# Kernel optimization log

Measured on AMD Instinct MI355X. Metric: run time of the kernel, lower is better.

Reference implementation:

```python
import jax, jax.numpy as jnp
import numpy as np

EMBED_DIM = 1280
NUM_HEADS = 20
HEAD_DIM = EMBED_DIM // NUM_HEADS
ENC_LEN = 8192
SCALE = float(HEAD_DIM ** -0.5)


def setup_inputs() -> dict:
    key = jax.random.key(0)
    ks = jax.random.split(key, 7)
    s = 0.02
    return {
        "hidden_states": jax.random.normal(ks[0], (1, 1, EMBED_DIM), dtype=jnp.float32),
        "cross_k_cache": jax.random.normal(ks[1], (1, NUM_HEADS, ENC_LEN, HEAD_DIM), dtype=jnp.float32),
        "cross_v_cache": jax.random.normal(ks[2], (1, NUM_HEADS, ENC_LEN, HEAD_DIM), dtype=jnp.float32),
        "q_w": jax.random.normal(ks[3], (EMBED_DIM, EMBED_DIM), dtype=jnp.float32) * s,
        "q_b": jax.random.normal(ks[4], (EMBED_DIM,), dtype=jnp.float32) * s,
        "out_w": jax.random.normal(ks[5], (EMBED_DIM, EMBED_DIM), dtype=jnp.float32) * s,
        "out_b": jax.random.normal(ks[6], (EMBED_DIM,), dtype=jnp.float32) * s,
    }


def reference(hidden_states, cross_k_cache, cross_v_cache, q_w, q_b, out_w, out_b):
    # q_proj (torch Linear: x @ W.T + b), then scale
    q = hidden_states @ q_w.T + q_b                       # [1,1,E]
    q = q * jnp.asarray(SCALE, q.dtype)
    q = q.reshape(1, 1, NUM_HEADS, HEAD_DIM).transpose(0, 2, 1, 3)  # [1,H,1,Dh]
    # attention scores over cached keys: [1,H,1,L]
    attn = jnp.einsum("bhqd,bhld->bhql", q, cross_k_cache)
    attn = jax.nn.softmax(attn, axis=-1)
    # weighted sum of values: [1,H,1,Dh]
    out = jnp.einsum("bhql,bhld->bhqd", attn, cross_v_cache)
    out = out.transpose(0, 2, 1, 3).reshape(1, 1, EMBED_DIM)
    return out @ out_w.T + out_b
```

## Files before the change

### kernel.cpp

```cpp
#include <hip/hip_runtime.h>
#include <math.h>

#define EMBED 1280
#define NHEAD 20
#define HDIM 64
#define LENC 8192
#define CHUNK 128
#define NBLK (LENC / CHUNK)
#define NREC 256
#define PREC 72
#define QSCALE 0.125f

__global__ __launch_bounds__(256) void matvec_row(
    const float* __restrict__ W, const float* __restrict__ x,
    const float* __restrict__ b, float* __restrict__ y, float scale) {
  int row = blockIdx.x;
  int t = threadIdx.x;
  int w = t >> 6, lane = t & 63;
  const float4* Wr = reinterpret_cast<const float4*>(W + (size_t)row * EMBED);
  const float4* x4 = reinterpret_cast<const float4*>(x);
  float4 wv = Wr[t], xv = x4[t];
  float acc = wv.x * xv.x + wv.y * xv.y + wv.z * xv.z + wv.w * xv.w;
  if (t < 64) {
    float4 wv2 = Wr[256 + t], xv2 = x4[256 + t];
    acc += wv2.x * xv2.x + wv2.y * xv2.y + wv2.z * xv2.z + wv2.w * xv2.w;
  }
#pragma unroll
  for (int msk = 32; msk > 0; msk >>= 1) acc += __shfl_xor(acc, msk);
  __shared__ float red[4];
  if (lane == 0) red[w] = acc;
  __syncthreads();
  if (t == 0) y[row] = scale * (red[0] + red[1] + red[2] + red[3] + b[row]);
}

__global__ __launch_bounds__(256) void attn_partial(
    const float* __restrict__ K, const float* __restrict__ V,
    const float* __restrict__ q, float* __restrict__ part) {
  int blk = blockIdx.x;
  int h = blk / NBLK;
  int c = blk % NBLK;
  int tid = threadIdx.x;
  int w = tid >> 6;
  int lane = tid & 63;
  int grp = lane >> 4;
  int l16 = lane & 15;

  size_t row0 = (size_t)c * CHUNK + (size_t)w * 32;
  const float4* Kh4 = reinterpret_cast<const float4*>(K + (size_t)h * LENC * HDIM) + row0 * 16;
  const float4* Vh4 = reinterpret_cast<const float4*>(V + (size_t)h * LENC * HDIM) + row0 * 16;
  float4 qv = reinterpret_cast<const float4*>(q + h * HDIM)[l16];

  float4 kreg[8], vreg[8];
#pragma unroll
  for (int it = 0; it < 8; ++it) kreg[it] = Kh4[(it * 4 + grp) * 16 + l16];
#pragma unroll
  for (int it = 0; it < 8; ++it) vreg[it] = Vh4[(it * 4 + grp) * 16 + l16];

  float s[8];
#pragma unroll
  for (int it = 0; it < 8; ++it) {
    float t = kreg[it].x * qv.x + kreg[it].y * qv.y + kreg[it].z * qv.z + kreg[it].w * qv.w;
    t += __shfl_xor(t, 1);
    t += __shfl_xor(t, 2);
    t += __shfl_xor(t, 4);
    t += __shfl_xor(t, 8);
    s[it] = t;
  }

  float m = s[0];
#pragma unroll
  for (int it = 1; it < 8; ++it) m = fmaxf(m, s[it]);
  m = fmaxf(m, __shfl_xor(m, 16));
  m = fmaxf(m, __shfl_xor(m, 32));

  float e[8], ssum = 0.f;
#pragma unroll
  for (int it = 0; it < 8; ++it) { e[it] = expf(s[it] - m); ssum += e[it]; }
  ssum += __shfl_xor(ssum, 16);
  ssum += __shfl_xor(ssum, 32);

  float4 o = make_float4(0.f, 0.f, 0.f, 0.f);
#pragma unroll
  for (int it = 0; it < 8; ++it) {
    o.x += e[it] * vreg[it].x;
    o.y += e[it] * vreg[it].y;
    o.z += e[it] * vreg[it].z;
    o.w += e[it] * vreg[it].w;
  }
#pragma unroll
  for (int msk = 16; msk <= 32; msk <<= 1) {
    o.x += __shfl_xor(o.x, msk);
    o.y += __shfl_xor(o.y, msk);
    o.z += __shfl_xor(o.z, msk);
    o.w += __shfl_xor(o.w, msk);
  }

  float* p = part + (size_t)(h * NREC + c * 4 + w) * PREC;
  if (grp == 0) {
    if (l16 == 0) { p[0] = m; p[1] = ssum; }
    reinterpret_cast<float4*>(p + 4)[l16] = o;
  }
}

__global__ __launch_bounds__(256) void attn_combine(
    const float* __restrict__ part, float* __restrict__ attn_out) {
  int h = blockIdx.x;
  int tid = threadIdx.x;
  int w = tid >> 6, lane = tid & 63;
  const float* p = part + (size_t)h * NREC * PREC;

  __shared__ float fsh[NREC];
  __shared__ float redM[4], redS[4];
  __shared__ float osum[4][HDIM];

  float mt = p[tid * PREC];
  float st = p[tid * PREC + 1];
  float m = mt;
#pragma unroll
  for (int msk = 32; msk > 0; msk >>= 1) m = fmaxf(m, __shfl_xor(m, msk));
  if (lane == 0) redM[w] = m;
  __syncthreads();
  float Mg = fmaxf(fmaxf(redM[0], redM[1]), fmaxf(redM[2], redM[3]));

  float f = expf(mt - Mg);
  fsh[tid] = f;
  float sc = st * f;
#pragma unroll
  for (int msk = 32; msk > 0; msk >>= 1) sc += __shfl_xor(sc, msk);
  if (lane == 0) redS[w] = sc;
  __syncthreads();
  float Sg = redS[0] + redS[1] + redS[2] + redS[3];

  float o = 0.f;
#pragma unroll
  for (int r = 0; r < 64; ++r) {
    int rec = w * 64 + r;
    o += fsh[rec] * p[rec * PREC + 4 + lane];
  }
  osum[w][lane] = o;
  __syncthreads();
  if (w == 0) {
    float oo = osum[0][lane] + osum[1][lane] + osum[2][lane] + osum[3][lane];
    attn_out[h * HDIM + lane] = oo / Sg;
  }
}


extern "C" void kernel_launch(void* const* d_in, const int* in_sizes, int n_in,
                              void* d_out, int out_size, void* d_ws, size_t ws_size,
                              hipStream_t stream) {
  const float* hs    = (const float*)d_in[0];
  const float* Kc    = (const float*)d_in[1];
  const float* Vc    = (const float*)d_in[2];
  const float* q_w   = (const float*)d_in[3];
  const float* q_b   = (const float*)d_in[4];
  const float* out_w = (const float*)d_in[5];
  const float* out_b = (const float*)d_in[6];
  float* out = (float*)d_out;

  float* ws = (float*)d_ws;
  float* qv       = ws;
  float* attn_out = ws + EMBED;
  float* part     = ws + 2 * EMBED;

  matvec_row<<<EMBED, 256, 0, stream>>>(q_w, hs, q_b, qv, QSCALE);
  attn_partial<<<NHEAD * NBLK, 256, 0, stream>>>(Kc, Vc, qv, part);
  attn_combine<<<NHEAD, 256, 0, stream>>>(part, attn_out);
  matvec_row<<<EMBED, 256, 0, stream>>>(out_w, attn_out, out_b, out, 1.0f);
}
```

Before: 29.30 us.

## Fuse attention combine into output projection with atomic-counter grid sync

Merges the per-head softmax combine kernel into the output-projection matvec kernel, removing one kernel launch. The first 20 blocks do the combine and signal through a global atomic counter. Every block prefetches its weight row, then spin-waits on the counter before reading attn_out. This depends on the combine blocks being scheduled while other blocks spin, which is a deadlock risk in general and adds spin-wait and atomic overhead.

```diff
diff --git a/kernel.cpp b/kernel.cpp
--- a/kernel.cpp
+++ b/kernel.cpp
@@ -11,9 +11,12 @@
 #define PREC 72
 #define QSCALE 0.125f
 
-__global__ __launch_bounds__(256) void matvec_row(
+__global__ __launch_bounds__(256) void matvec_qproj(
     const float* __restrict__ W, const float* __restrict__ x,
-    const float* __restrict__ b, float* __restrict__ y, float scale) {
+    const float* __restrict__ b, float* __restrict__ y,
+    int* __restrict__ done) {
+  if (blockIdx.x == 0 && threadIdx.x == 0)
+    __hip_atomic_store(done, 0, __ATOMIC_RELAXED, __HIP_MEMORY_SCOPE_AGENT);
   int row = blockIdx.x;
   int t = threadIdx.x;
   int w = t >> 6, lane = t & 63;
@@ -30,7 +33,7 @@
   __shared__ float red[4];
   if (lane == 0) red[w] = acc;
   __syncthreads();
-  if (t == 0) y[row] = scale * (red[0] + red[1] + red[2] + red[3] + b[row]);
+  if (t == 0) y[row] = QSCALE * (red[0] + red[1] + red[2] + red[3] + b[row]);
 }
 
 __global__ __launch_bounds__(256) void attn_partial(
@@ -102,47 +105,88 @@
   }
 }
 
-__global__ __launch_bounds__(256) void attn_combine(
-    const float* __restrict__ part, float* __restrict__ attn_out) {
-  int h = blockIdx.x;
-  int tid = threadIdx.x;
-  int w = tid >> 6, lane = tid & 63;
-  const float* p = part + (size_t)h * NREC * PREC;
-
-  __shared__ float fsh[NREC];
-  __shared__ float redM[4], redS[4];
-  __shared__ float osum[4][HDIM];
-
-  float mt = p[tid * PREC];
-  float st = p[tid * PREC + 1];
-  float m = mt;
-#pragma unroll
-  for (int msk = 32; msk > 0; msk >>= 1) m = fmaxf(m, __shfl_xor(m, msk));
-  if (lane == 0) redM[w] = m;
+__global__ __launch_bounds__(256) void combine_outproj(
+    const float* __restrict__ part, const float* __restrict__ W,
+    const float* __restrict__ b, float* __restrict__ attn_out,
+    int* __restrict__ done, float* __restrict__ out) {
+  int row = blockIdx.x;
+  int t = threadIdx.x;
+  int w = t >> 6, lane = t & 63;
+
+  const float4* Wr = reinterpret_cast<const float4*>(W + (size_t)row * EMBED);
+  float4 wv = Wr[t];
+  float4 wv2 = make_float4(0.f, 0.f, 0.f, 0.f);
+  if (t < 64) wv2 = Wr[256 + t];
+
+  __shared__ float red[4];
+
+  if (row < NHEAD) {
+    __shared__ float fsh[NREC];
+    __shared__ float redM[4], redS[4];
+    __shared__ float osum[4][HDIM];
+    const float* p = part + (size_t)row * NREC * PREC;
+    float mt = p[t * PREC];
+    float st = p[t * PREC + 1];
+    float m = mt;
+#pragma unroll
+    for (int msk = 32; msk > 0; msk >>= 1) m = fmaxf(m, __shfl_xor(m, msk));
+    if (lane == 0) redM[w] = m;
+    __syncthreads();
+    float Mg = fmaxf(fmaxf(redM[0], redM[1]), fmaxf(redM[2], redM[3]));
+    float f = expf(mt - Mg);
+    fsh[t] = f;
+    float sc = st * f;
+#pragma unroll
+    for (int msk = 32; msk > 0; msk >>= 1) sc += __shfl_xor(sc, msk);
+    if (lane == 0) redS[w] = sc;
+    __syncthreads();
+    float Sg = redS[0] + redS[1] + redS[2] + redS[3];
+
+    float o = 0.f;
+#pragma unroll 4
+    for (int r = 0; r < 64; ++r) {
+      int rec = w * 64 + r;
+      o += fsh[rec] * p[rec * PREC + 4 + lane];
+    }
+    osum[w][lane] = o;
+    __syncthreads();
+    if (w == 0) {
+      float oo = (osum[0][lane] + osum[1][lane] + osum[2][lane] + osum[3][lane]) / Sg;
+      __hip_atomic_store(&attn_out[row * HDIM + lane], oo, __ATOMIC_RELAXED,
+                         __HIP_MEMORY_SCOPE_AGENT);
+    }
+    __syncthreads();
+    if (t == 0)
+      __hip_atomic_fetch_add(done, 1, __ATOMIC_RELEASE, __HIP_MEMORY_SCOPE_AGENT);
+  }
+
+  if (t == 0) {
+    while (__hip_atomic_load(done, __ATOMIC_RELAXED, __HIP_MEMORY_SCOPE_AGENT) < NHEAD)
+      __builtin_amdgcn_s_sleep(2);
+  }
   __syncthreads();
-  float Mg = fmaxf(fmaxf(redM[0], redM[1]), fmaxf(redM[2], redM[3]));
-
-  float f = expf(mt - Mg);
-  fsh[tid] = f;
-  float sc = st * f;
-#pragma unroll
-  for (int msk = 32; msk > 0; msk >>= 1) sc += __shfl_xor(sc, msk);
-  if (lane == 0) redS[w] = sc;
+
+  float acc;
+  {
+    float x0 = __hip_atomic_load(&attn_out[4 * t + 0], __ATOMIC_RELAXED, __HIP_MEMORY_SCOPE_AGENT);
+    float x1 = __hip_atomic_load(&attn_out[4 * t + 1], __ATOMIC_RELAXED, __HIP_MEMORY_SCOPE_AGENT);
+    float x2 = __hip_atomic_load(&attn_out[4 * t + 2], __ATOMIC_RELAXED, __HIP_MEMORY_SCOPE_AGENT);
+    float x3 = __hip_atomic_load(&attn_out[4 * t + 3], __ATOMIC_RELAXED, __HIP_MEMORY_SCOPE_AGENT);
+    acc = wv.x * x0 + wv.y * x1 + wv.z * x2 + wv.w * x3;
+  }
+  if (t < 64) {
+    int base = 1024 + 4 * t;
+    float x0 = __hip_atomic_load(&attn_out[base + 0], __ATOMIC_RELAXED, __HIP_MEMORY_SCOPE_AGENT);
+    float x1 = __hip_atomic_load(&attn_out[base + 1], __ATOMIC_RELAXED, __HIP_MEMORY_SCOPE_AGENT);
+    float x2 = __hip_atomic_load(&attn_out[base + 2], __ATOMIC_RELAXED, __HIP_MEMORY_SCOPE_AGENT);
+    float x3 = __hip_atomic_load(&attn_out[base + 3], __ATOMIC_RELAXED, __HIP_MEMORY_SCOPE_AGENT);
+    acc += wv2.x * x0 + wv2.y * x1 + wv2.z * x2 + wv2.w * x3;
+  }
+#pragma unroll
+  for (int msk = 32; msk > 0; msk >>= 1) acc += __shfl_xor(acc, msk);
+  if (lane == 0) red[w] = acc;
   __syncthreads();
-  float Sg = redS[0] + redS[1] + redS[2] + redS[3];
-
-  float o = 0.f;
-#pragma unroll
-  for (int r = 0; r < 64; ++r) {
-    int rec = w * 64 + r;
-    o += fsh[rec] * p[rec * PREC + 4 + lane];
-  }
-  osum[w][lane] = o;
-  __syncthreads();
-  if (w == 0) {
-    float oo = osum[0][lane] + osum[1][lane] + osum[2][lane] + osum[3][lane];
-    attn_out[h * HDIM + lane] = oo / Sg;
-  }
+  if (t == 0) out[row] = red[0] + red[1] + red[2] + red[3] + b[row];
 }
 
 
@@ -159,12 +203,12 @@
   float* out = (float*)d_out;
 
   float* ws = (float*)d_ws;
-  float* qv       = ws;
-  float* attn_out = ws + EMBED;
-  float* part     = ws + 2 * EMBED;
-
-  matvec_row<<<EMBED, 256, 0, stream>>>(q_w, hs, q_b, qv, QSCALE);
+  int*   done     = (int*)ws;
+  float* qv       = ws + 32;
+  float* attn_out = ws + 32 + EMBED;
+  float* part     = ws + 32 + 2 * EMBED;
+
+  matvec_qproj<<<EMBED, 256, 0, stream>>>(q_w, hs, q_b, qv, done);
   attn_partial<<<NHEAD * NBLK, 256, 0, stream>>>(Kc, Vc, qv, part);
-  attn_combine<<<NHEAD, 256, 0, stream>>>(part, attn_out);
-  matvec_row<<<EMBED, 256, 0, stream>>>(out_w, attn_out, out_b, out, 1.0f);
-}
+  combine_outproj<<<EMBED, 256, 0, stream>>>(part, out_w, out_b, attn_out, done, out);
+}
```

Result: slower. 36.46 us (+24.5%).
